# Kernel tuning notes

Hardware: AMD Instinct MI355X
Metric: run time of the kernel (lower is better)

## Reference

```python
import jax, jax.numpy as jnp
import numpy as np
from jax import lax

T, D_IN, D_OUT = 8192, 4096, 4096
N_ADAPT, RANK = 8, 16


def setup_inputs() -> dict:
    key = jax.random.key(0)
    ks = jax.random.split(key, 6)
    x = jax.random.normal(ks[0], (T, D_IN), jnp.float32)
    weight_indices = jax.random.randint(ks[1], (T,), 0, N_ADAPT, jnp.int64 if jax.config.jax_enable_x64 else jnp.int32)
    W_base = jax.random.normal(ks[2], (D_OUT, D_IN), jnp.float32) * 0.02
    A_buffer = jax.random.normal(ks[3], (N_ADAPT, D_IN, RANK), jnp.float32) * 0.02
    B_buffer = jax.random.normal(ks[4], (N_ADAPT, RANK, D_OUT), jnp.float32) * 0.02
    DeltaW = jax.random.normal(ks[5], (N_ADAPT, D_IN, D_OUT), jnp.float32) * 0.02
    return {"x": x, "weight_indices": weight_indices, "W_base": W_base,
            "A_buffer": A_buffer, "B_buffer": B_buffer, "DeltaW": DeltaW}


def _ldmm(indices, x, A, B, D):
    """Per-token adapter matmul: out[t] = x[t] @ (DeltaW[j] + A[j] @ B[j]), j = indices[t].
    Grouped by adapter via masked GEMMs (fixed small adapter count), jit-friendly."""
    n_adapt = A.shape[0]
    acc0 = jnp.zeros((x.shape[0], D.shape[2]), x.dtype)

    def body(acc, inp):
        a_id, A_a, B_a, D_a = inp
        mask = (indices == a_id)[:, None]
        xm = jnp.where(mask, x, jnp.zeros((), x.dtype))  # [T, in]
        W_eff = D_a + A_a @ B_a                          # [in, out]
        return acc + xm @ W_eff, None

    acc, _ = lax.scan(body, acc0, (jnp.arange(n_adapt), A, B, D))
    return acc


def reference(x, weight_indices, W_base, A_buffer, B_buffer, DeltaW):
    base = x @ W_base.T                                   # ColumnParallelLinear
    delta = _ldmm(weight_indices, x, A_buffer, B_buffer, DeltaW)
    # NOTE: source has `base_output = +output` (unary plus, likely a typo for `+=`);
    # we implement the intended fused semantics base + ldmm.
    return base + delta
```

## Files before the change

kernel.cpp:

```cpp
#include <hip/hip_runtime.h>


#define T_TOKENS 8192
#define DIM 4096
#define NADAPT 8
#define RANK 16

#define BM2 256
#define BN2 256
#define MAXT2 40
#define GRIDX2 (MAXT2 * 16)

#define BM1 128
#define MAXT1 72

typedef __attribute__((ext_vector_type(8))) short bf16x8;
typedef __attribute__((ext_vector_type(4))) float f32x4;

__device__ __forceinline__ unsigned short f2bf(float f) {
  union { float f; unsigned u; } v; v.f = f;
  unsigned r = v.u + 0x7FFFu + ((v.u >> 16) & 1u);
  return (unsigned short)(r >> 16);
}

__device__ __forceinline__ void gload_lds16(const void* g, void* l) {
  __builtin_amdgcn_global_load_lds(
      (const __attribute__((address_space(1))) void*)g,
      (__attribute__((address_space(3))) void*)l, 16, 0, 0);
}

template <int N> __device__ __forceinline__ void vmwait() {
  if constexpr (N == 0)       asm volatile("s_waitcnt vmcnt(0)" ::: "memory");
  else if constexpr (N == 4)  asm volatile("s_waitcnt vmcnt(4)" ::: "memory");
  else if constexpr (N == 8)  asm volatile("s_waitcnt vmcnt(8)" ::: "memory");
  else                        asm volatile("s_waitcnt vmcnt(10)" ::: "memory");
}

__global__ void prep_kernel(const int* __restrict__ idx, int* __restrict__ perm,
                            int* __restrict__ meta, int padm) {
  __shared__ int s_cnt[NADAPT];
  __shared__ int s_padoff[NADAPT + 1];
  __shared__ int s_wsum[16];
  const int tid = threadIdx.x;
  const int lane = tid & 63;
  const int wave = tid >> 6;

  if (tid < NADAPT) s_cnt[tid] = 0;
  __syncthreads();
  for (int t = tid; t < T_TOKENS; t += 1024) atomicAdd(&s_cnt[idx[t]], 1);
  __syncthreads();

  if (tid == 0) {
    int off = 0, nt = 0;
    for (int j = 0; j < NADAPT; ++j) {
      meta[j] = s_cnt[j];
      s_padoff[j] = off;
      const int c = s_cnt[j];
      const int ntj = (c + padm - 1) / padm;
      for (int i = 0; i < ntj; ++i) {
        meta[32 + 3 * nt + 0] = j;
        meta[32 + 3 * nt + 1] = off + i * padm;
        meta[32 + 3 * nt + 2] = min(padm, c - i * padm);
        ++nt;
      }
      off += ntj * padm;
    }
    s_padoff[NADAPT] = off;
    meta[17] = nt;
    for (int j = 0; j <= NADAPT; ++j) meta[8 + j] = s_padoff[j];
  }
  __syncthreads();

  const int total_pad = s_padoff[NADAPT];
  for (int t = tid; t < total_pad; t += 1024) perm[t] = -1;
  __syncthreads();

  for (int j = 0; j < NADAPT; ++j) {
    int base = s_padoff[j];
    for (int c0 = 0; c0 < T_TOKENS; c0 += 1024) {
      const int t = c0 + tid;
      const int flag = (idx[t] == j) ? 1 : 0;
      const unsigned long long bal = __ballot(flag);
      const int wpos = __popcll(bal & ((1ULL << lane) - 1ULL));
      if (lane == 0) s_wsum[wave] = __popcll(bal);
      __syncthreads();
      int woff = 0, ctot = 0;
      for (int w = 0; w < 16; ++w) {
        const int v = s_wsum[w];
        if (w < wave) woff += v;
        ctot += v;
      }
      if (flag) perm[base + woff + wpos] = t;
      base += ctot;
      __syncthreads();
    }
  }
}

__global__ void convert_x_kernel(const float* __restrict__ x,
                                 unsigned short* __restrict__ xb) {
  const long long i = (long long)blockIdx.x * 256 + threadIdx.x;
  const float4* x4 = (const float4*)x;
  const float4 a = x4[2 * i];
  const float4 b = x4[2 * i + 1];
  uint4 o;
  o.x = (unsigned)f2bf(a.x) | ((unsigned)f2bf(a.y) << 16);
  o.y = (unsigned)f2bf(a.z) | ((unsigned)f2bf(a.w) << 16);
  o.z = (unsigned)f2bf(b.x) | ((unsigned)f2bf(b.y) << 16);
  o.w = (unsigned)f2bf(b.z) | ((unsigned)f2bf(b.w) << 16);
  ((uint4*)xb)[i] = o;
}

__global__ __launch_bounds__(256) void build_wtot_kernel(
    const float* __restrict__ Wb, const float* __restrict__ Am,
    const float* __restrict__ Bm, const float* __restrict__ DW,
    unsigned short* __restrict__ Wt, int j0) {
  const int jj = blockIdx.z;
  const int j = j0 + jj;
  const int i0 = blockIdx.x << 6;
  const int o0 = blockIdx.y << 6;
  __shared__ float Dl[64 * 64];
  __shared__ float Alt[16][68];
  __shared__ float Bl[16][68];
  const int tid = threadIdx.x;

  const float* dwp = DW + ((size_t)j * DIM + i0) * DIM + o0;
#pragma unroll
  for (int q = 0; q < 4; ++q) {
    const int lin = q * 256 + tid;
    const int i = lin >> 4;
    const int o4 = (lin & 15) << 2;
    const float4 v = *(const float4*)(dwp + (size_t)i * DIM + o4);
    const int iq = i >> 2, ie = i & 3;
#pragma unroll
    for (int k = 0; k < 4; ++k) {
      const int o = o4 + k;
      Dl[o * 64 + (((iq ^ (o & 15)) << 2) | ie)] = ((const float*)&v)[k];
    }
  }
  {
    const int ai = tid >> 2, r4 = (tid & 3) << 2;
    const float4 v = *(const float4*)(Am + ((size_t)j * DIM + i0 + ai) * RANK + r4);
#pragma unroll
    for (int k = 0; k < 4; ++k) Alt[r4 + k][ai] = ((const float*)&v)[k];
  }
  {
    const int br = tid >> 4, bo4 = (tid & 15) << 2;
    const float4 v = *(const float4*)(Bm + ((size_t)j * RANK + br) * DIM + o0 + bo4);
    *(float4*)&Bl[br][bo4] = v;
  }
  __syncthreads();

  const int to = (tid >> 4) << 2;
  const int ti = (tid & 15) << 2;
  float acc[4][4];

#pragma unroll
  for (int m = 0; m < 4; ++m) {
    const int o = to + m;
    const float4 w = *(const float4*)(Wb + (size_t)(o0 + o) * DIM + i0 + ti);
    const float4 d = *(const float4*)&Dl[o * 64 + (((ti >> 2) ^ (o & 15)) << 2)];
    acc[m][0] = w.x + d.x; acc[m][1] = w.y + d.y;
    acc[m][2] = w.z + d.z; acc[m][3] = w.w + d.w;
  }
#pragma unroll
  for (int r = 0; r < RANK; ++r) {
    const float4 av = *(const float4*)&Alt[r][ti];
    const float4 bv = *(const float4*)&Bl[r][to];
#pragma unroll
    for (int m = 0; m < 4; ++m) {
      const float b = ((const float*)&bv)[m];
      acc[m][0] += b * av.x; acc[m][1] += b * av.y;
      acc[m][2] += b * av.z; acc[m][3] += b * av.w;
    }
  }
#pragma unroll
  for (int m = 0; m < 4; ++m) {
    const int o = to + m;
    const unsigned lo = (unsigned)f2bf(acc[m][0]) | ((unsigned)f2bf(acc[m][1]) << 16);
    const unsigned hi = (unsigned)f2bf(acc[m][2]) | ((unsigned)f2bf(acc[m][3]) << 16);
    uint2 pk; pk.x = lo; pk.y = hi;
    *(uint2*)(Wt + ((size_t)jj * DIM + o0 + o) * DIM + i0 + ti) = pk;
  }
}

template <int BUF, int KK, int MQ, int VME, int SGRP, int SOP, int SKH, bool DOST>
__device__ __forceinline__ void do_phase(
    char* smem, int tid, int stile,
    const unsigned short* const* aB, const unsigned short* const* bB,
    const int* aoff, const int* boff, bf16x8* bfr, f32x4 (*acc)[4]) {
  const int grp = (BUF * 2 + KK) * 16384;
  if constexpr (MQ == 0) {
#pragma unroll
    for (int n = 0; n < 4; ++n)
      bfr[n] = *(const bf16x8*)(smem + 65536 + grp + boff[n]);
  }
  bf16x8 afr[4];
#pragma unroll
  for (int i = 0; i < 4; ++i)
    afr[i] = *(const bf16x8*)(smem + grp + aoff[MQ * 4 + i]);
  if constexpr (DOST) {
    const unsigned short* const* bs = SOP ? bB : aB;
#pragma unroll
    for (int q = 0; q < 2; ++q)
      gload_lds16(bs[q] + stile * 64 + SKH * 32,
                  smem + SOP * 65536 + SGRP * 16384 + q * 8192 + tid * 16);
  }
  __builtin_amdgcn_s_barrier();
  __builtin_amdgcn_s_setprio(1);
#pragma unroll
  for (int i = 0; i < 4; ++i)
#pragma unroll
    for (int n = 0; n < 4; ++n)
      acc[MQ * 4 + i][n] =
          __builtin_amdgcn_mfma_f32_16x16x32_bf16(afr[i], bfr[n], acc[MQ * 4 + i][n], 0, 0, 0);
  __builtin_amdgcn_s_setprio(0);
  vmwait<VME>();
  __builtin_amdgcn_s_barrier();
}

template <int SGRP, int SOP, int SKH>
__device__ __forceinline__ void do_stage(
    char* smem, int tid, int stile,
    const unsigned short* const* aB, const unsigned short* const* bB) {
  const unsigned short* const* bs = SOP ? bB : aB;
#pragma unroll
  for (int q = 0; q < 2; ++q)
    gload_lds16(bs[q] + stile * 64 + SKH * 32,
                smem + SOP * 65536 + SGRP * 16384 + q * 8192 + tid * 16);
}

__global__ __launch_bounds__(512, 2) void gemm8_kernel(
    const unsigned short* __restrict__ xb, const unsigned short* __restrict__ Wt,
    const int* __restrict__ perm, const int* __restrict__ meta,
    float* __restrict__ out, int j0, int npp) {
  extern __shared__ char smem[];
  const int ntiles = meta[17];
  const int flat = blockIdx.x;
  const int swz = (flat & 7) * (GRIDX2 / 8) + (flat >> 3);
  const int mt = swz >> 4;
  const int nt = swz & 15;
  if (mt >= ntiles) return;
  const int adapter = meta[32 + 3 * mt];
  if (adapter < j0 || adapter >= j0 + npp) return;
  const int slot = adapter - j0;
  const int pbase = meta[32 + 3 * mt + 1];
  const int nbase = nt << 8;

  const int tid = threadIdx.x;
  const int lane = tid & 63;
  const int wave = tid >> 6;
  const int wr = wave >> 2, wc = wave & 3;
  const int fr = lane & 15, kg = lane >> 4;

  int aoff[8], boff[4];
#pragma unroll
  for (int m = 0; m < 8; ++m) {
    const int row = wr * 128 + m * 16 + fr;
    const int r = row >> 1, hf = row & 1;
    const int c = ((hf << 2) | kg) ^ (r & 7);
    aoff[m] = r * 128 + c * 16;
  }
#pragma unroll
  for (int n = 0; n < 4; ++n) {
    const int row = wc * 64 + n * 16 + fr;
    const int r = row >> 1, hf = row & 1;
    const int c = ((hf << 2) | kg) ^ (r & 7);
    boff[n] = r * 128 + c * 16;
  }

  const unsigned short* aB[2];
  const unsigned short* bB[2];
#pragma unroll
  for (int q = 0; q < 2; ++q) {
    const int L = q * 512 + tid;
    const int r = L >> 3, c = L & 7;
    const int s = c ^ (r & 7);
    const int grow = 2 * r + (s >> 2);
    const int gk = (s & 3) << 3;
    int pr = perm[pbase + grow];
    if (pr < 0) pr = 0;
    aB[q] = xb + (size_t)pr * DIM + gk;
    bB[q] = Wt + ((size_t)slot * DIM + nbase + grow) * DIM + gk;
  }

  const f32x4 zero = {0.f, 0.f, 0.f, 0.f};
  f32x4 acc[8][4];
#pragma unroll
  for (int m = 0; m < 8; ++m)
#pragma unroll
    for (int n = 0; n < 4; ++n) acc[m][n] = zero;
  bf16x8 bfr[4];

  do_stage<0, 0, 0>(smem, tid, 0, aB, bB);
  do_stage<0, 1, 0>(smem, tid, 0, aB, bB);
  do_stage<1, 0, 1>(smem, tid, 0, aB, bB);
  do_stage<1, 1, 1>(smem, tid, 0, aB, bB);
  do_stage<2, 0, 0>(smem, tid, 1, aB, bB);
  do_stage<2, 1, 0>(smem, tid, 1, aB, bB);
  vmwait<8>();
  __builtin_amdgcn_s_barrier();

  for (int it = 0; it < 31; ++it) {
    const int t1 = 2 * it + 1, t2 = 2 * it + 2, t3 = 2 * it + 3;
    do_phase<0, 0, 0, 10, 3, 0, 1, true>(smem, tid, t1, aB, bB, aoff, boff, bfr, acc);
    do_phase<0, 0, 1, 8,  3, 1, 1, true>(smem, tid, t1, aB, bB, aoff, boff, bfr, acc);
    do_phase<0, 1, 0, 10, 0, 0, 0, true>(smem, tid, t2, aB, bB, aoff, boff, bfr, acc);
    do_phase<0, 1, 1, 8,  0, 1, 0, true>(smem, tid, t2, aB, bB, aoff, boff, bfr, acc);
    do_phase<1, 0, 0, 10, 1, 0, 1, true>(smem, tid, t2, aB, bB, aoff, boff, bfr, acc);
    do_phase<1, 0, 1, 8,  1, 1, 1, true>(smem, tid, t2, aB, bB, aoff, boff, bfr, acc);
    do_phase<1, 1, 0, 10, 2, 0, 0, true>(smem, tid, t3, aB, bB, aoff, boff, bfr, acc);
    do_phase<1, 1, 1, 8,  2, 1, 0, true>(smem, tid, t3, aB, bB, aoff, boff, bfr, acc);
  }
  do_phase<0, 0, 0, 10, 3, 0, 1, true >(smem, tid, 63, aB, bB, aoff, boff, bfr, acc);
  do_phase<0, 0, 1, 8,  3, 1, 1, true >(smem, tid, 63, aB, bB, aoff, boff, bfr, acc);
  do_phase<0, 1, 0, 8,  0, 0, 0, false>(smem, tid, 0,  aB, bB, aoff, boff, bfr, acc);
  do_phase<0, 1, 1, 4,  0, 0, 0, false>(smem, tid, 0,  aB, bB, aoff, boff, bfr, acc);
  do_phase<1, 0, 0, 4,  0, 0, 0, false>(smem, tid, 0,  aB, bB, aoff, boff, bfr, acc);
  do_phase<1, 0, 1, 0,  0, 0, 0, false>(smem, tid, 0,  aB, bB, aoff, boff, bfr, acc);
  do_phase<1, 1, 0, 0,  0, 0, 0, false>(smem, tid, 0,  aB, bB, aoff, boff, bfr, acc);
  do_phase<1, 1, 1, 0,  0, 0, 0, false>(smem, tid, 0,  aB, bB, aoff, boff, bfr, acc);

#pragma unroll
  for (int m = 0; m < 8; ++m) {
#pragma unroll
    for (int t = 0; t < 4; ++t) {
      const int rt = wr * 128 + m * 16 + kg * 4 + t;
      const int pr = perm[pbase + rt];
      if (pr < 0) continue;
      float* orow = out + (size_t)pr * DIM + nbase + wc * 64;
#pragma unroll
      for (int n = 0; n < 4; ++n) orow[n * 16 + fr] = acc[m][n][t];
    }
  }
}

template <bool USE_XB>
__global__ __launch_bounds__(256) void gemm_kernel(
    const unsigned short* __restrict__ xb, const float* __restrict__ xf,
    const unsigned short* __restrict__ Wt,
    const int* __restrict__ perm, const int* __restrict__ meta,
    float* __restrict__ out, int j0, int npp) {
  const int ntiles = meta[17];
  const int mt = blockIdx.x;
  if (mt >= ntiles) return;
  const int adapter = meta[32 + 3 * mt];
  if (adapter < j0 || adapter >= j0 + npp) return;
  const int slot = adapter - j0;
  const int nt = blockIdx.y;
  const int pbase = meta[32 + 3 * mt + 1];
  const int nbase = nt << 7;

  __shared__ __align__(16) unsigned short As[BM1 * 64];
  __shared__ __align__(16) unsigned short Bs[BM1 * 64];

  const int tid = threadIdx.x;
  const int lane = tid & 63;
  const int wave = tid >> 6;

  const unsigned short* aSrcB[4];
  const float* aSrcF[4];
  const unsigned short* bSrc[4];
  unsigned short* aDst[4];
  unsigned short* bDst[4];
#pragma unroll
  for (int q = 0; q < 4; ++q) {
    const int c = wave * 4 + q;
    const int r = c * 8 + (lane >> 3);
    int pr = perm[pbase + r];
    if (pr < 0) pr = 0;
    if (USE_XB) aSrcB[q] = xb + (size_t)pr * DIM + (lane & 7) * 8;
    else        aSrcF[q] = xf + (size_t)pr * DIM + (lane & 7) * 8;
    bSrc[q] = Wt + ((size_t)slot * DIM + nbase + r) * DIM + (lane & 7) * 8;
    aDst[q] = As + c * 512;
    bDst[q] = Bs + c * 512;
  }

  const int wr = wave >> 1, wc = wave & 1;
  const int fr = lane & 15, kg = lane >> 4;

  const f32x4 zero = {0.f, 0.f, 0.f, 0.f};
  f32x4 acc[4][4];
#pragma unroll
  for (int m = 0; m < 4; ++m)
#pragma unroll
    for (int n = 0; n < 4; ++n) acc[m][n] = zero;

  for (int k0 = 0; k0 < DIM; k0 += 64) {
    if (USE_XB) {
#pragma unroll
      for (int q = 0; q < 4; ++q) gload_lds16(aSrcB[q] + k0, aDst[q]);
    } else {
#pragma unroll
      for (int q = 0; q < 4; ++q) {
        const float4 va = *(const float4*)(aSrcF[q] + k0);
        const float4 vb = *(const float4*)(aSrcF[q] + k0 + 4);
        union { bf16x8 v; unsigned short s[8]; } u;
        u.s[0] = f2bf(va.x); u.s[1] = f2bf(va.y); u.s[2] = f2bf(va.z); u.s[3] = f2bf(va.w);
        u.s[4] = f2bf(vb.x); u.s[5] = f2bf(vb.y); u.s[6] = f2bf(vb.z); u.s[7] = f2bf(vb.w);
        *(bf16x8*)(aDst[q] + lane * 8) = u.v;
      }
    }
#pragma unroll
    for (int q = 0; q < 4; ++q) gload_lds16(bSrc[q] + k0, bDst[q]);
    __syncthreads();
#pragma unroll
    for (int kk = 0; kk < 2; ++kk) {
      bf16x8 a[4], b[4];
#pragma unroll
      for (int m = 0; m < 4; ++m)
        a[m] = *(const bf16x8*)(&As[(wr * 64 + m * 16 + fr) * 64 + kk * 32 + kg * 8]);
#pragma unroll
      for (int n = 0; n < 4; ++n)
        b[n] = *(const bf16x8*)(&Bs[(wc * 64 + n * 16 + fr) * 64 + kk * 32 + kg * 8]);
#pragma unroll
      for (int m = 0; m < 4; ++m)
#pragma unroll
        for (int n = 0; n < 4; ++n)
          acc[m][n] = __builtin_amdgcn_mfma_f32_16x16x32_bf16(a[m], b[n], acc[m][n], 0, 0, 0);
    }
    __syncthreads();
  }

#pragma unroll
  for (int m = 0; m < 4; ++m) {
#pragma unroll
    for (int t = 0; t < 4; ++t) {
      const int rt = wr * 64 + m * 16 + kg * 4 + t;
      const int pr = perm[pbase + rt];
      if (pr < 0) continue;
      float* orow = out + (size_t)pr * DIM + nbase + wc * 64;
#pragma unroll
      for (int n = 0; n < 4; ++n) orow[n * 16 + fr] = acc[m][n][t];
    }
  }
}

extern "C" void kernel_launch(void* const* d_in, const int* in_sizes, int n_in,
                              void* d_out, int out_size, void* d_ws, size_t ws_size,
                              hipStream_t stream) {
  const float* x  = (const float*)d_in[0];
  const int* widx = (const int*)d_in[1];
  const float* Wb = (const float*)d_in[2];
  const float* Am = (const float*)d_in[3];
  const float* Bm = (const float*)d_in[4];
  const float* DW = (const float*)d_in[5];
  float* out = (float*)d_out;

  const size_t XB_BYTES = (size_t)T_TOKENS * DIM * 2;
  const size_t WT1_BYTES = (size_t)DIM * DIM * 2;
  const size_t PM_BYTES = 16384 * sizeof(int) + 4096;

  int npp = 0;
  bool use_xb = true;
  for (int cand = NADAPT; cand >= 1; cand >>= 1) {
    if (XB_BYTES + (size_t)cand * WT1_BYTES + PM_BYTES <= ws_size) { npp = cand; break; }
  }
  if (npp == 0) { npp = 1; use_xb = false; }

  bool use8 = use_xb &&
      (hipFuncSetAttribute((const void*)gemm8_kernel,
                           hipFuncAttributeMaxDynamicSharedMemorySize, 131072) == hipSuccess);

  char* ws = (char*)d_ws;
  unsigned short* xb = (unsigned short*)ws;
  unsigned short* Wt = (unsigned short*)(ws + (use_xb ? XB_BYTES : 0));
  char* tail = (char*)Wt + (size_t)npp * WT1_BYTES;
  int* perm = (int*)tail;
  int* meta = (int*)(tail + 16384 * sizeof(int));

  prep_kernel<<<dim3(1), dim3(1024), 0, stream>>>(widx, perm, meta, use8 ? BM2 : BM1);
  if (use_xb)
    convert_x_kernel<<<dim3(T_TOKENS * DIM / (256 * 8)), dim3(256), 0, stream>>>(x, xb);

  const int passes = NADAPT / npp;
  for (int p = 0; p < passes; ++p) {
    const int j0 = p * npp;
    build_wtot_kernel<<<dim3(DIM / 64, DIM / 64, npp), dim3(256), 0, stream>>>(
        Wb, Am, Bm, DW, Wt, j0);
    if (use8)
      gemm8_kernel<<<dim3(GRIDX2), dim3(512), 131072, stream>>>(
          xb, Wt, perm, meta, out, j0, npp);
    else if (use_xb)
      gemm_kernel<true><<<dim3(MAXT1, DIM / 128), dim3(256), 0, stream>>>(
          xb, nullptr, Wt, perm, meta, out, j0, npp);
    else
      gemm_kernel<false><<<dim3(MAXT1, DIM / 128), dim3(256), 0, stream>>>(
          nullptr, x, Wt, perm, meta, out, j0, npp);
  }
}
```

Measured before the change: 703.0 us.

## Shrink grouped GEMM tile to 256x128 with 8 waves and 4-phase pipeline

Replaces the 256x256 tile GEMM with a 256x128 tile variant. Each of the 8 waves computes a 64x64 sub-tile using a 4x4 accumulator, and the grid doubles to 32 column tiles. LDS use drops from 128KB to 96KB. The pipeline is restructured into 4 phases per pair of K-tiles, each staging 3 loads. The aim is to cut register and LDS pressure, allowing more occupancy and better load balance across many small adapter tiles, at the cost of lower arithmetic intensity and more re-reads of A.

```diff
diff --git a/kernel.cpp b/kernel.cpp
--- a/kernel.cpp
+++ b/kernel.cpp
@@ -7,9 +7,8 @@
 #define RANK 16
 
 #define BM2 256
-#define BN2 256
 #define MAXT2 40
-#define GRIDX2 (MAXT2 * 16)
+#define GRIDX3 (MAXT2 * 32)
 
 #define BM1 128
 #define MAXT1 72
@@ -30,10 +29,10 @@
 }
 
 template <int N> __device__ __forceinline__ void vmwait() {
-  if constexpr (N == 0)       asm volatile("s_waitcnt vmcnt(0)" ::: "memory");
-  else if constexpr (N == 4)  asm volatile("s_waitcnt vmcnt(4)" ::: "memory");
-  else if constexpr (N == 8)  asm volatile("s_waitcnt vmcnt(8)" ::: "memory");
-  else                        asm volatile("s_waitcnt vmcnt(10)" ::: "memory");
+  if constexpr (N == 0)      asm volatile("s_waitcnt vmcnt(0)" ::: "memory");
+  else if constexpr (N == 3) asm volatile("s_waitcnt vmcnt(3)" ::: "memory");
+  else if constexpr (N == 6) asm volatile("s_waitcnt vmcnt(6)" ::: "memory");
+  else                       asm volatile("s_waitcnt vmcnt(8)" ::: "memory");
 }
 
 __global__ void prep_kernel(const int* __restrict__ idx, int* __restrict__ perm,
@@ -184,27 +183,24 @@
   }
 }
 
-template <int BUF, int KK, int MQ, int VME, int SGRP, int SOP, int SKH, bool DOST>
-__device__ __forceinline__ void do_phase(
+template <int BUF, int KH, int VME, int SBUF, int SKH, bool DOST>
+__device__ __forceinline__ void phase4(
     char* smem, int tid, int stile,
-    const unsigned short* const* aB, const unsigned short* const* bB,
-    const int* aoff, const int* boff, bf16x8* bfr, f32x4 (*acc)[4]) {
-  const int grp = (BUF * 2 + KK) * 16384;
-  if constexpr (MQ == 0) {
-#pragma unroll
-    for (int n = 0; n < 4; ++n)
-      bfr[n] = *(const bf16x8*)(smem + 65536 + grp + boff[n]);
-  }
-  bf16x8 afr[4];
-#pragma unroll
-  for (int i = 0; i < 4; ++i)
-    afr[i] = *(const bf16x8*)(smem + grp + aoff[MQ * 4 + i]);
+    const unsigned short* const* aB, const unsigned short* bB0,
+    const int* aoff, const int* boff, f32x4 (*acc)[4]) {
+  const int ga = (BUF * 2 + KH) * 16384;
+  const int gb = 65536 + (BUF * 2 + KH) * 8192;
+  bf16x8 afr[4], bfr[4];
+#pragma unroll
+  for (int i = 0; i < 4; ++i) afr[i] = *(const bf16x8*)(smem + ga + aoff[i]);
+#pragma unroll
+  for (int n = 0; n < 4; ++n) bfr[n] = *(const bf16x8*)(smem + gb + boff[n]);
   if constexpr (DOST) {
-    const unsigned short* const* bs = SOP ? bB : aB;
-#pragma unroll
-    for (int q = 0; q < 2; ++q)
-      gload_lds16(bs[q] + stile * 64 + SKH * 32,
-                  smem + SOP * 65536 + SGRP * 16384 + q * 8192 + tid * 16);
+    const int sga = (SBUF * 2 + SKH) * 16384;
+    const int sgb = 65536 + (SBUF * 2 + SKH) * 8192;
+    gload_lds16(aB[0] + stile * 64 + SKH * 32, smem + sga + tid * 16);
+    gload_lds16(aB[1] + stile * 64 + SKH * 32, smem + sga + 8192 + tid * 16);
+    gload_lds16(bB0 + stile * 64 + SKH * 32, smem + sgb + tid * 16);
   }
   __builtin_amdgcn_s_barrier();
   __builtin_amdgcn_s_setprio(1);
@@ -212,51 +208,51 @@
   for (int i = 0; i < 4; ++i)
 #pragma unroll
     for (int n = 0; n < 4; ++n)
-      acc[MQ * 4 + i][n] =
-          __builtin_amdgcn_mfma_f32_16x16x32_bf16(afr[i], bfr[n], acc[MQ * 4 + i][n], 0, 0, 0);
+      acc[i][n] = __builtin_amdgcn_mfma_f32_16x16x32_bf16(afr[i], bfr[n], acc[i][n], 0, 0, 0);
   __builtin_amdgcn_s_setprio(0);
   vmwait<VME>();
   __builtin_amdgcn_s_barrier();
 }
 
-template <int SGRP, int SOP, int SKH>
-__device__ __forceinline__ void do_stage(
+template <int SBUF, int SKH>
+__device__ __forceinline__ void stage3(
     char* smem, int tid, int stile,
-    const unsigned short* const* aB, const unsigned short* const* bB) {
-  const unsigned short* const* bs = SOP ? bB : aB;
-#pragma unroll
-  for (int q = 0; q < 2; ++q)
-    gload_lds16(bs[q] + stile * 64 + SKH * 32,
-                smem + SOP * 65536 + SGRP * 16384 + q * 8192 + tid * 16);
-}
-
-__global__ __launch_bounds__(512, 2) void gemm8_kernel(
+    const unsigned short* const* aB, const unsigned short* bB0) {
+  const int sga = (SBUF * 2 + SKH) * 16384;
+  const int sgb = 65536 + (SBUF * 2 + SKH) * 8192;
+  gload_lds16(aB[0] + stile * 64 + SKH * 32, smem + sga + tid * 16);
+  gload_lds16(aB[1] + stile * 64 + SKH * 32, smem + sga + 8192 + tid * 16);
+  gload_lds16(bB0 + stile * 64 + SKH * 32, smem + sgb + tid * 16);
+}
+
+__global__ __launch_bounds__(512, 2) void gemm4p_kernel(
     const unsigned short* __restrict__ xb, const unsigned short* __restrict__ Wt,
     const int* __restrict__ perm, const int* __restrict__ meta,
     float* __restrict__ out, int j0, int npp) {
   extern __shared__ char smem[];
   const int ntiles = meta[17];
   const int flat = blockIdx.x;
-  const int swz = (flat & 7) * (GRIDX2 / 8) + (flat >> 3);
-  const int mt = swz >> 4;
-  const int nt = swz & 15;
+  const int swz = (flat & 7) * (GRIDX3 / 8) + (flat >> 3);
+  const int mt = swz >> 5;
+  const int nt = swz & 31;
   if (mt >= ntiles) return;
   const int adapter = meta[32 + 3 * mt];
   if (adapter < j0 || adapter >= j0 + npp) return;
   const int slot = adapter - j0;
   const int pbase = meta[32 + 3 * mt + 1];
-  const int nbase = nt << 8;
+  const int nbase = nt << 7;
 
   const int tid = threadIdx.x;
   const int lane = tid & 63;
   const int wave = tid >> 6;
-  const int wr = wave >> 2, wc = wave & 3;
+  const int wr = wave >> 1;
+  const int wc = wave & 1;
   const int fr = lane & 15, kg = lane >> 4;
 
-  int aoff[8], boff[4];
-#pragma unroll
-  for (int m = 0; m < 8; ++m) {
-    const int row = wr * 128 + m * 16 + fr;
+  int aoff[4], boff[4];
+#pragma unroll
+  for (int m = 0; m < 4; ++m) {
+    const int row = wr * 64 + m * 16 + fr;
     const int r = row >> 1, hf = row & 1;
     const int c = ((hf << 2) | kg) ^ (r & 7);
     aoff[m] = r * 128 + c * 16;
@@ -270,7 +266,7 @@
   }
 
   const unsigned short* aB[2];
-  const unsigned short* bB[2];
+  const unsigned short* bB0;
 #pragma unroll
   for (int q = 0; q < 2; ++q) {
     const int L = q * 512 + tid;
@@ -281,51 +277,44 @@
     int pr = perm[pbase + grow];
     if (pr < 0) pr = 0;
     aB[q] = xb + (size_t)pr * DIM + gk;
-    bB[q] = Wt + ((size_t)slot * DIM + nbase + grow) * DIM + gk;
+  }
+  {
+    const int r = tid >> 3, c = tid & 7;
+    const int s = c ^ (r & 7);
+    const int grow = 2 * r + (s >> 2);
+    const int gk = (s & 3) << 3;
+    bB0 = Wt + ((size_t)slot * DIM + nbase + grow) * DIM + gk;
   }
 
   const f32x4 zero = {0.f, 0.f, 0.f, 0.f};
-  f32x4 acc[8][4];
-#pragma unroll
-  for (int m = 0; m < 8; ++m)
+  f32x4 acc[4][4];
+#pragma unroll
+  for (int m = 0; m < 4; ++m)
 #pragma unroll
     for (int n = 0; n < 4; ++n) acc[m][n] = zero;
-  bf16x8 bfr[4];
-
-  do_stage<0, 0, 0>(smem, tid, 0, aB, bB);
-  do_stage<0, 1, 0>(smem, tid, 0, aB, bB);
-  do_stage<1, 0, 1>(smem, tid, 0, aB, bB);
-  do_stage<1, 1, 1>(smem, tid, 0, aB, bB);
-  do_stage<2, 0, 0>(smem, tid, 1, aB, bB);
-  do_stage<2, 1, 0>(smem, tid, 1, aB, bB);
-  vmwait<8>();
+
+  stage3<0, 0>(smem, tid, 0, aB, bB0);
+  stage3<0, 1>(smem, tid, 0, aB, bB0);
+  stage3<1, 0>(smem, tid, 1, aB, bB0);
+  vmwait<6>();
   __builtin_amdgcn_s_barrier();
 
-  for (int it = 0; it < 31; ++it) {
-    const int t1 = 2 * it + 1, t2 = 2 * it + 2, t3 = 2 * it + 3;
-    do_phase<0, 0, 0, 10, 3, 0, 1, true>(smem, tid, t1, aB, bB, aoff, boff, bfr, acc);
-    do_phase<0, 0, 1, 8,  3, 1, 1, true>(smem, tid, t1, aB, bB, aoff, boff, bfr, acc);
-    do_phase<0, 1, 0, 10, 0, 0, 0, true>(smem, tid, t2, aB, bB, aoff, boff, bfr, acc);
-    do_phase<0, 1, 1, 8,  0, 1, 0, true>(smem, tid, t2, aB, bB, aoff, boff, bfr, acc);
-    do_phase<1, 0, 0, 10, 1, 0, 1, true>(smem, tid, t2, aB, bB, aoff, boff, bfr, acc);
-    do_phase<1, 0, 1, 8,  1, 1, 1, true>(smem, tid, t2, aB, bB, aoff, boff, bfr, acc);
-    do_phase<1, 1, 0, 10, 2, 0, 0, true>(smem, tid, t3, aB, bB, aoff, boff, bfr, acc);
-    do_phase<1, 1, 1, 8,  2, 1, 0, true>(smem, tid, t3, aB, bB, aoff, boff, bfr, acc);
-  }
-  do_phase<0, 0, 0, 10, 3, 0, 1, true >(smem, tid, 63, aB, bB, aoff, boff, bfr, acc);
-  do_phase<0, 0, 1, 8,  3, 1, 1, true >(smem, tid, 63, aB, bB, aoff, boff, bfr, acc);
-  do_phase<0, 1, 0, 8,  0, 0, 0, false>(smem, tid, 0,  aB, bB, aoff, boff, bfr, acc);
-  do_phase<0, 1, 1, 4,  0, 0, 0, false>(smem, tid, 0,  aB, bB, aoff, boff, bfr, acc);
-  do_phase<1, 0, 0, 4,  0, 0, 0, false>(smem, tid, 0,  aB, bB, aoff, boff, bfr, acc);
-  do_phase<1, 0, 1, 0,  0, 0, 0, false>(smem, tid, 0,  aB, bB, aoff, boff, bfr, acc);
-  do_phase<1, 1, 0, 0,  0, 0, 0, false>(smem, tid, 0,  aB, bB, aoff, boff, bfr, acc);
-  do_phase<1, 1, 1, 0,  0, 0, 0, false>(smem, tid, 0,  aB, bB, aoff, boff, bfr, acc);
-
-#pragma unroll
-  for (int m = 0; m < 8; ++m) {
+  for (int s = 0; s < 31; ++s) {
+    phase4<0, 0, 6, 1, 1, true>(smem, tid, 2 * s + 1, aB, bB0, aoff, boff, acc);
+    phase4<0, 1, 6, 0, 0, true>(smem, tid, 2 * s + 2, aB, bB0, aoff, boff, acc);
+    phase4<1, 0, 6, 0, 1, true>(smem, tid, 2 * s + 2, aB, bB0, aoff, boff, acc);
+    phase4<1, 1, 6, 1, 0, true>(smem, tid, 2 * s + 3, aB, bB0, aoff, boff, acc);
+  }
+  phase4<0, 0, 6, 1, 1, true >(smem, tid, 63, aB, bB0, aoff, boff, acc);
+  phase4<0, 1, 3, 0, 0, false>(smem, tid, 0, aB, bB0, aoff, boff, acc);
+  phase4<1, 0, 0, 0, 0, false>(smem, tid, 0, aB, bB0, aoff, boff, acc);
+  phase4<1, 1, 0, 0, 0, false>(smem, tid, 0, aB, bB0, aoff, boff, acc);
+
+#pragma unroll
+  for (int m = 0; m < 4; ++m) {
 #pragma unroll
     for (int t = 0; t < 4; ++t) {
-      const int rt = wr * 128 + m * 16 + kg * 4 + t;
+      const int rt = wr * 64 + m * 16 + kg * 4 + t;
       const int pr = perm[pbase + rt];
       if (pr < 0) continue;
       float* orow = out + (size_t)pr * DIM + nbase + wc * 64;
@@ -458,9 +447,9 @@
   }
   if (npp == 0) { npp = 1; use_xb = false; }
 
-  bool use8 = use_xb &&
-      (hipFuncSetAttribute((const void*)gemm8_kernel,
-                           hipFuncAttributeMaxDynamicSharedMemorySize, 131072) == hipSuccess);
+  bool use4 = use_xb &&
+      (hipFuncSetAttribute((const void*)gemm4p_kernel,
+                           hipFuncAttributeMaxDynamicSharedMemorySize, 98304) == hipSuccess);
 
   char* ws = (char*)d_ws;
   unsigned short* xb = (unsigned short*)ws;
@@ -469,7 +458,7 @@
   int* perm = (int*)tail;
   int* meta = (int*)(tail + 16384 * sizeof(int));
 
-  prep_kernel<<<dim3(1), dim3(1024), 0, stream>>>(widx, perm, meta, use8 ? BM2 : BM1);
+  prep_kernel<<<dim3(1), dim3(1024), 0, stream>>>(widx, perm, meta, use4 ? BM2 : BM1);
   if (use_xb)
     convert_x_kernel<<<dim3(T_TOKENS * DIM / (256 * 8)), dim3(256), 0, stream>>>(x, xb);
 
@@ -478,8 +467,8 @@
     const int j0 = p * npp;
     build_wtot_kernel<<<dim3(DIM / 64, DIM / 64, npp), dim3(256), 0, stream>>>(
         Wb, Am, Bm, DW, Wt, j0);
-    if (use8)
-      gemm8_kernel<<<dim3(GRIDX2), dim3(512), 131072, stream>>>(
+    if (use4)
+      gemm4p_kernel<<<dim3(GRIDX3), dim3(512), 98304, stream>>>(
           xb, Wt, perm, meta, out, j0, npp);
     else if (use_xb)
       gemm_kernel<true><<<dim3(MAXT1, DIM / 128), dim3(256), 0, stream>>>(
```

Result: slower. 819.6 us (+16.6%).
